# Optimization experiments

Hardware: AMD Instinct MI355X
Metric: run time of the kernel (lower is better)

## Reference

```python
import jax, jax.numpy as jnp
import numpy as np

NUM_NODES = 50000
NUM_GRAPHS = 50
HID = 128
GFD = 2
L = 4
EPS_MSG = 1e-7


def layer_norm(x, g, b, eps=1e-5):
    mu = jnp.mean(x, axis=-1, keepdims=True)
    xc = x - mu
    var = jnp.mean(xc * xc, axis=-1, keepdims=True)
    return xc * jax.lax.rsqrt(var + eps) * g + b


def gen_conv(x, src, dst, ea, t, W1, b1, g1, be1, W2, b2):
    # GENConv message: relu(x_j + edge_attr) + eps  -> [E, h]
    msg = jax.nn.relu(x[src] + ea) + EPS_MSG
    # per-destination, per-channel softmax weights of t*msg
    logits = msg * t
    m = jax.ops.segment_max(logits, dst, num_segments=NUM_NODES)
    m = jnp.where(jnp.isfinite(m), m, 0.0)  # isolated nodes -> -inf guard
    m = jax.lax.stop_gradient(m)
    ex = jnp.exp(logits - m[dst])
    s = jax.ops.segment_sum(ex, dst, num_segments=NUM_NODES)
    agg = jax.ops.segment_sum(ex * msg, dst, num_segments=NUM_NODES) / jnp.where(s > 0, s, 1.0)
    out = agg + x  # root residual inside GENConv
    # GENConv MLP: Linear(h,2h) -> LayerNorm -> ReLU -> Linear(2h,h)
    h = layer_norm(out @ W1 + b1, g1, be1)
    h = jax.nn.relu(h)
    return h @ W2 + b2


def forward(x, edge_index, edge_attr, graph_features, node_W, node_b, edge_W, edge_b,
            ts, W1s, b1s, g1s, be1s, W2s, b2s, ln_gs, ln_bs,
            head_W0, head_b0, head_W1, head_b1):
    src, dst = edge_index[0], edge_index[1]
    x = x @ node_W + node_b                 # node_encoder
    ea = edge_attr @ edge_W + edge_b        # edge_encoder
    # layers[0].conv applied directly (no pre-norm)
    x = gen_conv(x, src, dst, ea, ts[0], W1s[0], b1s[0], g1s[0], be1s[0], W2s[0], b2s[0])
    # remaining layers: res+ blocks: x = x + conv(act(norm(x)))
    for i in range(1, L):
        h = jax.nn.relu(layer_norm(x, ln_gs[i], ln_bs[i]))
        h = gen_conv(h, src, dst, ea, ts[i], W1s[i], b1s[i], g1s[i], be1s[i], W2s[i], b2s[i])
        x = x + h
    # final norm/act taken from layers[0]
    x = jax.nn.relu(layer_norm(x, ln_gs[0], ln_bs[0]))
    # dropout(p=0.1) is identity in eval mode
    # graph features broadcast to nodes (faithful reshape sequence)
    G = graph_features.shape[0]
    npg = x.shape[0] // G                   # nodes per graph
    t = jnp.repeat(graph_features.T[:, :, None], npg, axis=2)  # [gfd, G, npg]
    t = t.reshape(G, GFD, npg)              # row-major reinterpret (torch .view)
    t = jnp.transpose(t, (1, 0, 2)).reshape(GFD, G * npg)      # cat(unbind(0), dim=1)
    x = jnp.concatenate([x, t.T], axis=1)   # [N, h + gfd]
    x = jax.nn.relu(x @ head_W0 + head_b0)
    x = x @ head_W1 + head_b1
    return x


def setup_inputs() -> dict:
    key = jax.random.key(0)
    ks = jax.random.split(key, 32)
    E = 800000
    d_in, d_e = 64, 16

    def lin(k, fi, fo):
        return jax.random.normal(k, (fi, fo), jnp.float32) / np.sqrt(fi)

    inp = {
        'x': jax.random.normal(ks[0], (NUM_NODES, d_in), jnp.float32),
        'edge_index': jax.random.randint(ks[1], (2, E), 0, NUM_NODES, jnp.int64 if jax.config.jax_enable_x64 else jnp.int32),
        'edge_attr': jax.random.normal(ks[2], (E, d_e), jnp.float32),
        'graph_features': jax.random.normal(ks[3], (NUM_GRAPHS, GFD), jnp.float32),
        'node_W': lin(ks[4], d_in, HID), 'node_b': jnp.zeros((HID,), jnp.float32),
        'edge_W': lin(ks[5], d_e, HID), 'edge_b': jnp.zeros((HID,), jnp.float32),
        'ts': jnp.ones((L,), jnp.float32),
        'W1s': jnp.stack([lin(ks[6 + i], HID, 2 * HID) for i in range(L)]),
        'b1s': jnp.zeros((L, 2 * HID), jnp.float32),
        'g1s': jnp.ones((L, 2 * HID), jnp.float32),
        'be1s': jnp.zeros((L, 2 * HID), jnp.float32),
        'W2s': jnp.stack([lin(ks[10 + i], 2 * HID, HID) for i in range(L)]),
        'b2s': jnp.zeros((L, HID), jnp.float32),
        'ln_gs': jnp.ones((L, HID), jnp.float32),
        'ln_bs': jnp.zeros((L, HID), jnp.float32),
        'head_W0': lin(ks[14], HID + GFD, HID), 'head_b0': jnp.zeros((HID,), jnp.float32),
        'head_W1': lin(ks[15], HID, 1), 'head_b1': jnp.zeros((1,), jnp.float32),
    }
    return inp


def reference(x, edge_index, edge_attr, graph_features, node_W, node_b, edge_W, edge_b,
              ts, W1s, b1s, g1s, be1s, W2s, b2s, ln_gs, ln_bs,
              head_W0, head_b0, head_W1, head_b1):
    return forward(x, edge_index, edge_attr, graph_features, node_W, node_b, edge_W, edge_b,
                   ts, W1s, b1s, g1s, be1s, W2s, b2s, ln_gs, ln_bs,
                   head_W0, head_b0, head_W1, head_b1)
```

## Files before the change

kernel.cpp:

```cpp
#include <hip/hip_runtime.h>
#include <math.h>

#define EPS_MSG 1e-7f

typedef float v2f __attribute__((ext_vector_type(2)));
typedef float v4f __attribute__((ext_vector_type(4)));
typedef short bf16x8 __attribute__((ext_vector_type(8)));
typedef float f32x4 __attribute__((ext_vector_type(4)));
typedef unsigned short ush;

static __device__ inline v2f sp(float a) { v2f r; r.x = a; r.y = a; return r; }

__device__ inline unsigned short f2bf(float f) {
    union { float f; unsigned int i; } u; u.f = f;
    unsigned int b = u.i;
    return (unsigned short)((b + 0x7fffu + ((b >> 16) & 1u)) >> 16);
}
__device__ inline float bf2f(unsigned short h) {
    union { unsigned int i; float f; } u; u.i = ((unsigned int)h) << 16;
    return u.f;
}
__device__ inline v2f ubf2(unsigned int u) {
    union { unsigned int i; float f; } a, b;
    a.i = u << 16; b.i = u & 0xffff0000u;
    v2f r; r.x = a.f; r.y = b.f; return r;
}

__global__ void zero2_kernel(int* __restrict__ a, int* __restrict__ b, int n) {
    int i = blockIdx.x * 256 + threadIdx.x;
    if (i < n) { a[i] = 0; b[i] = 0; }
}

__global__ void deg_kernel(const int* __restrict__ ei, int* __restrict__ deg, int E) {
    int e = blockIdx.x * 256 + threadIdx.x;
    if (e < E) atomicAdd(&deg[ei[E + e]], 1);
}

__global__ __launch_bounds__(1024)
void scan1_kernel(const int* __restrict__ deg, int* __restrict__ offs,
                  int* __restrict__ bsum, int n) {
    __shared__ int sh[1024];
    int tid = threadIdx.x;
    int i = blockIdx.x * 1024 + tid;
    int v = (i < n) ? deg[i] : 0;
    sh[tid] = v;
    __syncthreads();
    for (int off = 1; off < 1024; off <<= 1) {
        int t = (tid >= off) ? sh[tid - off] : 0;
        __syncthreads();
        sh[tid] += t;
        __syncthreads();
    }
    if (i < n) offs[i] = sh[tid] - v;
    if (tid == 1023) bsum[blockIdx.x] = sh[tid];
}

__global__ __launch_bounds__(64)
void scan2_kernel(int* __restrict__ bsum, int nb) {
    int lane = threadIdx.x;
    int carry = 0;
    for (int base = 0; base < nb; base += 64) {
        int v = (base + lane < nb) ? bsum[base + lane] : 0;
        int incl = v;
#pragma unroll
        for (int off = 1; off < 64; off <<= 1) {
            int t = __shfl_up(incl, off, 64);
            if (lane >= off) incl += t;
        }
        if (base + lane < nb) bsum[base + lane] = incl - v + carry;
        carry += __shfl(incl, 63, 64);
    }
    if (lane == 0) bsum[nb] = carry;
}

__global__ void scan3_kernel(int* __restrict__ offs, const int* __restrict__ bsum, int n) {
    int i = blockIdx.x * 256 + threadIdx.x;
    if (i < n) offs[i] += bsum[i >> 10];
    else if (i == n) offs[n] = bsum[(n + 1023) >> 10];
}

__global__ void scatter_pos_kernel(const int* __restrict__ ei, const int* __restrict__ offs,
                                   int* __restrict__ fill, int* __restrict__ src_perm,
                                   int* __restrict__ eid_perm, int E) {
    int e = blockIdx.x * 256 + threadIdx.x;
    if (e >= E) return;
    int s = ei[e];
    int d = ei[E + e];
    int pos = offs[d] + atomicAdd(&fill[d], 1);
    src_perm[pos] = s;
    eid_perm[pos] = e;
}

__global__ void gather_attr_kernel(const float* __restrict__ edge_attr,
                                   const int* __restrict__ eid_perm,
                                   float* __restrict__ attr_perm, int E) {
    int idx = blockIdx.x * 256 + threadIdx.x;
    if (idx >= E * 4) return;
    int p = idx >> 2, c = idx & 3;
    int e = eid_perm[p];
    float4 v = *(const float4*)&edge_attr[(size_t)e * 16 + c * 4];
    *(float4*)&attr_perm[(size_t)p * 16 + c * 4] = v;
}

__global__ void wswz_kernel(const float* __restrict__ W, unsigned short* __restrict__ WH,
                            unsigned short* __restrict__ WL, int K, int Ncol, int total) {
    int idx = blockIdx.x * 256 + threadIdx.x;
    if (idx >= total) return;
    int j = idx & 7;
    int lane = (idx >> 3) & 63;
    int rest = idx >> 9;
    int ks = K >> 5;
    int kstep = rest % ks;
    int rest2 = rest / ks;
    int nc = Ncol >> 4;
    int c16 = rest2 % nc;
    int l = rest2 / nc;
    int k = kstep * 32 + (lane >> 4) * 8 + j;
    int n = c16 * 16 + (lane & 15);
    float v = W[(size_t)l * K * Ncol + (size_t)k * Ncol + n];
    unsigned short hi = f2bf(v);
    unsigned short lo = f2bf(v - bf2f(hi));
    WH[idx] = hi;
    WL[idx] = lo;
}

__global__ __launch_bounds__(256)
void encode_kernel(const float* __restrict__ x, const float* __restrict__ W,
                   const float* __restrict__ b, float* __restrict__ out,
                   unsigned short* __restrict__ xb, int N) {
    __shared__ __align__(16) float Xa[32][64];
    int tid = threadIdx.x;
    int node0 = blockIdx.x * 32;
    {
        int row = tid >> 3;
        int col = (tid & 7) * 8;
        float4 v0 = make_float4(0, 0, 0, 0), v1 = make_float4(0, 0, 0, 0);
        if (node0 + row < N) {
            const float* sp_ = &x[(size_t)(node0 + row) * 64 + col];
            v0 = *(const float4*)sp_;
            v1 = *(const float4*)(sp_ + 4);
        }
        *(float4*)&Xa[row][col] = v0;
        *(float4*)&Xa[row][col + 4] = v1;
    }
    __syncthreads();
    int tx = tid & 31, rg = tid >> 5;
    int c = tx * 4;
    v2f ba = *(const v2f*)&b[c];
    v2f bb = *(const v2f*)&b[c + 2];
    v2f acc[4][2];
#pragma unroll
    for (int i = 0; i < 4; ++i) { acc[i][0] = ba; acc[i][1] = bb; }
    for (int k = 0; k < 64; k += 4) {
        v4f W0 = *(const v4f*)&W[(k + 0) * 128 + c];
        v4f W1r = *(const v4f*)&W[(k + 1) * 128 + c];
        v4f W2r = *(const v4f*)&W[(k + 2) * 128 + c];
        v4f W3r = *(const v4f*)&W[(k + 3) * 128 + c];
#pragma unroll
        for (int i = 0; i < 4; ++i) {
            v4f xv = *(const v4f*)&Xa[rg * 4 + i][k];
            acc[i][0] = __builtin_elementwise_fma(sp(xv.x), W0.xy, acc[i][0]);
            acc[i][1] = __builtin_elementwise_fma(sp(xv.x), W0.zw, acc[i][1]);
            acc[i][0] = __builtin_elementwise_fma(sp(xv.y), W1r.xy, acc[i][0]);
            acc[i][1] = __builtin_elementwise_fma(sp(xv.y), W1r.zw, acc[i][1]);
            acc[i][0] = __builtin_elementwise_fma(sp(xv.z), W2r.xy, acc[i][0]);
            acc[i][1] = __builtin_elementwise_fma(sp(xv.z), W2r.zw, acc[i][1]);
            acc[i][0] = __builtin_elementwise_fma(sp(xv.w), W3r.xy, acc[i][0]);
            acc[i][1] = __builtin_elementwise_fma(sp(xv.w), W3r.zw, acc[i][1]);
        }
    }
#pragma unroll
    for (int i = 0; i < 4; ++i) {
        int row = node0 + rg * 4 + i;
        if (row < N) {
            float4 o = make_float4(acc[i][0].x, acc[i][0].y, acc[i][1].x, acc[i][1].y);
            *(float4*)&out[(size_t)row * 128 + c] = o;
            if (xb) {
                unsigned int u0 = (unsigned int)f2bf(o.x) | ((unsigned int)f2bf(o.y) << 16);
                unsigned int u1 = (unsigned int)f2bf(o.z) | ((unsigned int)f2bf(o.w) << 16);
                *(unsigned int*)&xb[(size_t)row * 128 + c] = u0;
                *(unsigned int*)&xb[(size_t)row * 128 + c + 2] = u1;
            }
        }
    }
}

__global__ __launch_bounds__(256)
void ln_relu_kernel(const float* __restrict__ x, const float* __restrict__ g,
                    const float* __restrict__ b, float* __restrict__ out,
                    unsigned short* __restrict__ gb, int N) {
    int lane = threadIdx.x & 63;
    int node = blockIdx.x * 4 + (threadIdx.x >> 6);
    if (node >= N) return;
    int c0 = lane * 2;
    float2 xv = *(const float2*)&x[(size_t)node * 128 + c0];
    float s = xv.x + xv.y;
    float q = xv.x * xv.x + xv.y * xv.y;
#pragma unroll
    for (int m = 1; m < 64; m <<= 1) { s += __shfl_xor(s, m, 64); q += __shfl_xor(q, m, 64); }
    float mu = s * (1.f / 128.f);
    float var = q * (1.f / 128.f) - mu * mu;
    float rs = rsqrtf(var + 1e-5f);
    float ox = fmaxf((xv.x - mu) * rs * g[c0] + b[c0], 0.f);
    float oy = fmaxf((xv.y - mu) * rs * g[c0 + 1] + b[c0 + 1], 0.f);
    float2 o; o.x = ox; o.y = oy;
    *(float2*)&out[(size_t)node * 128 + c0] = o;
    if (gb) {
        unsigned int u = (unsigned int)f2bf(ox) | ((unsigned int)f2bf(oy) << 16);
        *(unsigned int*)&gb[(size_t)node * 128 + c0] = u;
    }
}

__global__ __launch_bounds__(256)
void ln_relu_bf_kernel(const float* __restrict__ x, const float* __restrict__ g,
                       const float* __restrict__ b, unsigned short* __restrict__ outH,
                       unsigned short* __restrict__ outL, int N) {
    int lane = threadIdx.x & 63;
    int node = blockIdx.x * 4 + (threadIdx.x >> 6);
    if (node >= N) return;
    int c0 = lane * 2;
    float2 xv = *(const float2*)&x[(size_t)node * 128 + c0];
    float s = xv.x + xv.y;
    float q = xv.x * xv.x + xv.y * xv.y;
#pragma unroll
    for (int m = 1; m < 64; m <<= 1) { s += __shfl_xor(s, m, 64); q += __shfl_xor(q, m, 64); }
    float mu = s * (1.f / 128.f);
    float var = q * (1.f / 128.f) - mu * mu;
    float rs = rsqrtf(var + 1e-5f);
    float ox = fmaxf((xv.x - mu) * rs * g[c0] + b[c0], 0.f);
    float oy = fmaxf((xv.y - mu) * rs * g[c0 + 1] + b[c0 + 1], 0.f);
    unsigned short hx = f2bf(ox), hy = f2bf(oy);
    unsigned short lx = f2bf(ox - bf2f(hx)), ly = f2bf(oy - bf2f(hy));
    *(unsigned int*)&outH[(size_t)node * 128 + c0] = (unsigned int)hx | ((unsigned int)hy << 16);
    *(unsigned int*)&outL[(size_t)node * 128 + c0] = (unsigned int)lx | ((unsigned int)ly << 16);
}

template <int BF>
__global__ __launch_bounds__(128, 8)
void conv_kernel(const float* __restrict__ pre, const unsigned short* __restrict__ preb,
                 const float* __restrict__ attr_perm,
                 const int* __restrict__ src_perm, const int* __restrict__ offs,
                 const float* __restrict__ edge_W, const float* __restrict__ edge_b,
                 const float* __restrict__ ts, int layer,
                 unsigned short* __restrict__ convH, unsigned short* __restrict__ convL, int N) {
    int lane = threadIdx.x & 63;
    int node = blockIdx.x * 2 + (threadIdx.x >> 6);
    if (node >= N) return;
    int c0 = lane * 2;
    v2f wE[16];
#pragma unroll
    for (int k = 0; k < 16; ++k) {
        wE[k].x = edge_W[k * 128 + c0];
        wE[k].y = edge_W[k * 128 + c0 + 1];
    }
    v2f eb; eb.x = edge_b[c0]; eb.y = edge_b[c0 + 1];
    float t = ts[layer];
    int i0 = offs[node], i1 = offs[node + 1];
    v2f xself = *(const v2f*)&pre[(size_t)node * 128 + c0];
    float sx = 0.f, sy = 0.f, wx = 0.f, wy = 0.f;
    int i = i0;
    for (; i + 3 < i1; i += 4) {
        int iu = __builtin_amdgcn_readfirstlane(i);
        int sn0 = src_perm[iu];
        int sn1 = src_perm[iu + 1];
        int sn2 = src_perm[iu + 2];
        int sn3 = src_perm[iu + 3];
        v2f x0, x1, x2, x3;
        if (BF) {
            unsigned int u0 = *(const unsigned int*)&preb[(size_t)sn0 * 128 + c0];
            unsigned int u1 = *(const unsigned int*)&preb[(size_t)sn1 * 128 + c0];
            unsigned int u2 = *(const unsigned int*)&preb[(size_t)sn2 * 128 + c0];
            unsigned int u3 = *(const unsigned int*)&preb[(size_t)sn3 * 128 + c0];
            x0 = ubf2(u0); x1 = ubf2(u1); x2 = ubf2(u2); x3 = ubf2(u3);
        } else {
            x0 = *(const v2f*)&pre[(size_t)sn0 * 128 + c0];
            x1 = *(const v2f*)&pre[(size_t)sn1 * 128 + c0];
            x2 = *(const v2f*)&pre[(size_t)sn2 * 128 + c0];
            x3 = *(const v2f*)&pre[(size_t)sn3 * 128 + c0];
        }
        const v4f* ar = (const v4f*)(attr_perm + (size_t)iu * 16);
        v2f ea0 = eb, ea1 = eb, ea2 = eb, ea3 = eb;
#pragma unroll
        for (int k = 0; k < 4; ++k) {
            v4f A0 = ar[k];
            v4f A1 = ar[4 + k];
            v4f A2 = ar[8 + k];
            v4f A3 = ar[12 + k];
            ea0 = __builtin_elementwise_fma(sp(A0.x), wE[4 * k + 0], ea0);
            ea1 = __builtin_elementwise_fma(sp(A1.x), wE[4 * k + 0], ea1);
            ea2 = __builtin_elementwise_fma(sp(A2.x), wE[4 * k + 0], ea2);
            ea3 = __builtin_elementwise_fma(sp(A3.x), wE[4 * k + 0], ea3);
            ea0 = __builtin_elementwise_fma(sp(A0.y), wE[4 * k + 1], ea0);
            ea1 = __builtin_elementwise_fma(sp(A1.y), wE[4 * k + 1], ea1);
            ea2 = __builtin_elementwise_fma(sp(A2.y), wE[4 * k + 1], ea2);
            ea3 = __builtin_elementwise_fma(sp(A3.y), wE[4 * k + 1], ea3);
            ea0 = __builtin_elementwise_fma(sp(A0.z), wE[4 * k + 2], ea0);
            ea1 = __builtin_elementwise_fma(sp(A1.z), wE[4 * k + 2], ea1);
            ea2 = __builtin_elementwise_fma(sp(A2.z), wE[4 * k + 2], ea2);
            ea3 = __builtin_elementwise_fma(sp(A3.z), wE[4 * k + 2], ea3);
            ea0 = __builtin_elementwise_fma(sp(A0.w), wE[4 * k + 3], ea0);
            ea1 = __builtin_elementwise_fma(sp(A1.w), wE[4 * k + 3], ea1);
            ea2 = __builtin_elementwise_fma(sp(A2.w), wE[4 * k + 3], ea2);
            ea3 = __builtin_elementwise_fma(sp(A3.w), wE[4 * k + 3], ea3);
        }
        float m0x = fmaxf(x0.x + ea0.x, 0.f) + EPS_MSG;
        float m0y = fmaxf(x0.y + ea0.y, 0.f) + EPS_MSG;
        float m1x = fmaxf(x1.x + ea1.x, 0.f) + EPS_MSG;
        float m1y = fmaxf(x1.y + ea1.y, 0.f) + EPS_MSG;
        float m2x = fmaxf(x2.x + ea2.x, 0.f) + EPS_MSG;
        float m2y = fmaxf(x2.y + ea2.y, 0.f) + EPS_MSG;
        float m3x = fmaxf(x3.x + ea3.x, 0.f) + EPS_MSG;
        float m3y = fmaxf(x3.y + ea3.y, 0.f) + EPS_MSG;
        float e0x = __expf(m0x * t), e0y = __expf(m0y * t);
        float e1x = __expf(m1x * t), e1y = __expf(m1y * t);
        float e2x = __expf(m2x * t), e2y = __expf(m2y * t);
        float e3x = __expf(m3x * t), e3y = __expf(m3y * t);
        sx += (e0x + e1x) + (e2x + e3x);
        sy += (e0y + e1y) + (e2y + e3y);
        wx = fmaf(e0x, m0x, wx); wx = fmaf(e1x, m1x, wx);
        wx = fmaf(e2x, m2x, wx); wx = fmaf(e3x, m3x, wx);
        wy = fmaf(e0y, m0y, wy); wy = fmaf(e1y, m1y, wy);
        wy = fmaf(e2y, m2y, wy); wy = fmaf(e3y, m3y, wy);
    }
    for (; i < i1; ++i) {
        int iu = __builtin_amdgcn_readfirstlane(i);
        int sn = src_perm[iu];
        const v4f* ar = (const v4f*)(attr_perm + (size_t)iu * 16);
        v2f xv;
        if (BF) {
            unsigned int u = *(const unsigned int*)&preb[(size_t)sn * 128 + c0];
            xv = ubf2(u);
        } else {
            xv = *(const v2f*)&pre[(size_t)sn * 128 + c0];
        }
        v2f ea = eb;
#pragma unroll
        for (int k = 0; k < 4; ++k) {
            v4f A0 = ar[k];
            ea = __builtin_elementwise_fma(sp(A0.x), wE[4 * k + 0], ea);
            ea = __builtin_elementwise_fma(sp(A0.y), wE[4 * k + 1], ea);
            ea = __builtin_elementwise_fma(sp(A0.z), wE[4 * k + 2], ea);
            ea = __builtin_elementwise_fma(sp(A0.w), wE[4 * k + 3], ea);
        }
        float mgx = fmaxf(xv.x + ea.x, 0.f) + EPS_MSG;
        float mgy = fmaxf(xv.y + ea.y, 0.f) + EPS_MSG;
        float ex = __expf(mgx * t), ey = __expf(mgy * t);
        sx += ex; sy += ey;
        wx = fmaf(ex, mgx, wx);
        wy = fmaf(ey, mgy, wy);
    }
    float ax = (sx > 0.f) ? wx / sx : 0.f;
    float ay = (sy > 0.f) ? wy / sy : 0.f;
    float ox = ax + xself.x;
    float oy = ay + xself.y;
    unsigned short hx = f2bf(ox), hy = f2bf(oy);
    unsigned short lx = f2bf(ox - bf2f(hx)), ly = f2bf(oy - bf2f(hy));
    *(unsigned int*)&convH[(size_t)node * 128 + c0] = (unsigned int)hx | ((unsigned int)hy << 16);
    *(unsigned int*)&convL[(size_t)node * 128 + c0] = (unsigned int)lx | ((unsigned int)ly << 16);
}

template <int RES>
__global__ __launch_bounds__(256)
void mlp_mfma(const unsigned short* __restrict__ convH, const unsigned short* __restrict__ convL,
              const unsigned short* __restrict__ W1H, const unsigned short* __restrict__ W1L,
              const float* __restrict__ b1, const float* __restrict__ g1, const float* __restrict__ be1,
              const unsigned short* __restrict__ W2H, const unsigned short* __restrict__ W2L,
              const float* __restrict__ b2, const float* __restrict__ xold,
              float* __restrict__ xnew, int N) {
    __shared__ __align__(16) char SH[33792];
    __shared__ float2 ps[4][32];
    ush (*XaH)[136] = (ush(*)[136])&SH[0];
    ush (*XaL)[136] = (ush(*)[136])&SH[8704];
    ush (*XhH)[264] = (ush(*)[264])&SH[0];
    ush (*XhL)[264] = (ush(*)[264])&SH[16896];
    int tid = threadIdx.x;
    int w = tid >> 6;
    int lane = tid & 63;
    int g = lane >> 4;
    int r = lane & 15;
    int node0 = blockIdx.x * 32;
    {
        int row = tid >> 3;
        int cb = (tid & 7) * 16;
        uint4 h0 = make_uint4(0, 0, 0, 0), h1 = h0, l0 = h0, l1 = h0;
        if (node0 + row < N) {
            const uint4* pH = (const uint4*)&convH[(size_t)(node0 + row) * 128 + cb];
            const uint4* pL = (const uint4*)&convL[(size_t)(node0 + row) * 128 + cb];
            h0 = pH[0]; h1 = pH[1];
            l0 = pL[0]; l1 = pL[1];
        }
        *(uint4*)&XaH[row][cb] = h0; *(uint4*)&XaH[row][cb + 8] = h1;
        *(uint4*)&XaL[row][cb] = l0; *(uint4*)&XaL[row][cb + 8] = l1;
    }
    __syncthreads();
    f32x4 acc1[2][4];
#pragma unroll
    for (int cf = 0; cf < 4; ++cf) {
        float bv = b1[(w * 4 + cf) * 16 + r];
        f32x4 iv; iv[0] = bv; iv[1] = bv; iv[2] = bv; iv[3] = bv;
        acc1[0][cf] = iv; acc1[1][cf] = iv;
    }
#pragma unroll
    for (int kstep = 0; kstep < 4; ++kstep) {
        int ko = kstep * 32 + g * 8;
        bf16x8 aH0 = *(const bf16x8*)&XaH[r][ko];
        bf16x8 aH1 = *(const bf16x8*)&XaH[16 + r][ko];
        bf16x8 aL0 = *(const bf16x8*)&XaL[r][ko];
        bf16x8 aL1 = *(const bf16x8*)&XaL[16 + r][ko];
#pragma unroll
        for (int cf = 0; cf < 4; ++cf) {
            int c16 = w * 4 + cf;
            bf16x8 bH = *(const bf16x8*)&W1H[(((size_t)c16 * 4 + kstep) * 64 + lane) * 8];
            bf16x8 bL = *(const bf16x8*)&W1L[(((size_t)c16 * 4 + kstep) * 64 + lane) * 8];
            acc1[0][cf] = __builtin_amdgcn_mfma_f32_16x16x32_bf16(aH0, bH, acc1[0][cf], 0, 0, 0);
            acc1[0][cf] = __builtin_amdgcn_mfma_f32_16x16x32_bf16(aH0, bL, acc1[0][cf], 0, 0, 0);
            acc1[0][cf] = __builtin_amdgcn_mfma_f32_16x16x32_bf16(aL0, bH, acc1[0][cf], 0, 0, 0);
            acc1[1][cf] = __builtin_amdgcn_mfma_f32_16x16x32_bf16(aH1, bH, acc1[1][cf], 0, 0, 0);
            acc1[1][cf] = __builtin_amdgcn_mfma_f32_16x16x32_bf16(aH1, bL, acc1[1][cf], 0, 0, 0);
            acc1[1][cf] = __builtin_amdgcn_mfma_f32_16x16x32_bf16(aL1, bH, acc1[1][cf], 0, 0, 0);
        }
    }
    {
        float s_[2][4], q_[2][4];
#pragma unroll
        for (int rf = 0; rf < 2; ++rf)
#pragma unroll
            for (int reg = 0; reg < 4; ++reg) {
                float s = 0.f, q = 0.f;
#pragma unroll
                for (int cf = 0; cf < 4; ++cf) {
                    float v = acc1[rf][cf][reg];
                    s += v; q += v * v;
                }
                s_[rf][reg] = s; q_[rf][reg] = q;
            }
#pragma unroll
        for (int m = 1; m < 16; m <<= 1) {
#pragma unroll
            for (int rf = 0; rf < 2; ++rf)
#pragma unroll
                for (int reg = 0; reg < 4; ++reg) {
                    s_[rf][reg] += __shfl_xor(s_[rf][reg], m, 64);
                    q_[rf][reg] += __shfl_xor(q_[rf][reg], m, 64);
                }
        }
        if (r == 0) {
#pragma unroll
            for (int rf = 0; rf < 2; ++rf)
#pragma unroll
                for (int reg = 0; reg < 4; ++reg)
                    ps[w][rf * 16 + g * 4 + reg] = make_float2(s_[rf][reg], q_[rf][reg]);
        }
    }
    __syncthreads();
    {
        float gv[4], bev[4];
#pragma unroll
        for (int cf = 0; cf < 4; ++cf) {
            gv[cf] = g1[(w * 4 + cf) * 16 + r];
            bev[cf] = be1[(w * 4 + cf) * 16 + r];
        }
#pragma unroll
        for (int rf = 0; rf < 2; ++rf)
#pragma unroll
            for (int reg = 0; reg < 4; ++reg) {
                int row = rf * 16 + g * 4 + reg;
                float2 t0 = ps[0][row], t1 = ps[1][row], t2 = ps[2][row], t3 = ps[3][row];
                float s = t0.x + t1.x + t2.x + t3.x;
                float q = t0.y + t1.y + t2.y + t3.y;
                float mu = s * (1.f / 256.f);
                float var = q * (1.f / 256.f) - mu * mu;
                float rs = rsqrtf(var + 1e-5f);
#pragma unroll
                for (int cf = 0; cf < 4; ++cf) {
                    float h = fmaxf((acc1[rf][cf][reg] - mu) * rs * gv[cf] + bev[cf], 0.f);
                    unsigned short hh = f2bf(h);
                    unsigned short hl = f2bf(h - bf2f(hh));
                    int col = (w * 4 + cf) * 16 + r;
                    XhH[row][col] = hh;
                    XhL[row][col] = hl;
                }
            }
    }
    __syncthreads();
    f32x4 acc2[2][2];
#pragma unroll
    for (int cf = 0; cf < 2; ++cf) {
        float bv = b2[(w * 2 + cf) * 16 + r];
        f32x4 iv; iv[0] = bv; iv[1] = bv; iv[2] = bv; iv[3] = bv;
        acc2[0][cf] = iv; acc2[1][cf] = iv;
    }
#pragma unroll
    for (int kstep = 0; kstep < 8; ++kstep) {
        int ko = kstep * 32 + g * 8;
        bf16x8 aH0 = *(const bf16x8*)&XhH[r][ko];
        bf16x8 aH1 = *(const bf16x8*)&XhH[16 + r][ko];
        bf16x8 aL0 = *(const bf16x8*)&XhL[r][ko];
        bf16x8 aL1 = *(const bf16x8*)&XhL[16 + r][ko];
#pragma unroll
        for (int cf = 0; cf < 2; ++cf) {
            int c16 = w * 2 + cf;
            bf16x8 bH = *(const bf16x8*)&W2H[(((size_t)c16 * 8 + kstep) * 64 + lane) * 8];
            bf16x8 bL = *(const bf16x8*)&W2L[(((size_t)c16 * 8 + kstep) * 64 + lane) * 8];
            acc2[0][cf] = __builtin_amdgcn_mfma_f32_16x16x32_bf16(aH0, bH, acc2[0][cf], 0, 0, 0);
            acc2[0][cf] = __builtin_amdgcn_mfma_f32_16x16x32_bf16(aH0, bL, acc2[0][cf], 0, 0, 0);
            acc2[0][cf] = __builtin_amdgcn_mfma_f32_16x16x32_bf16(aL0, bH, acc2[0][cf], 0, 0, 0);
            acc2[1][cf] = __builtin_amdgcn_mfma_f32_16x16x32_bf16(aH1, bH, acc2[1][cf], 0, 0, 0);
            acc2[1][cf] = __builtin_amdgcn_mfma_f32_16x16x32_bf16(aH1, bL, acc2[1][cf], 0, 0, 0);
            acc2[1][cf] = __builtin_amdgcn_mfma_f32_16x16x32_bf16(aL1, bH, acc2[1][cf], 0, 0, 0);
        }
    }
#pragma unroll
    for (int rf = 0; rf < 2; ++rf)
#pragma unroll
        for (int reg = 0; reg < 4; ++reg) {
            int row = node0 + rf * 16 + g * 4 + reg;
            if (row < N) {
#pragma unroll
                for (int cf = 0; cf < 2; ++cf) {
                    int col = (w * 2 + cf) * 16 + r;
                    float v = acc2[rf][cf][reg];
                    if (RES) v += xold[(size_t)row * 128 + col];
                    xnew[(size_t)row * 128 + col] = v;
                }
            }
        }
}

__global__ __launch_bounds__(256)
void head_mfma(const unsigned short* __restrict__ PREH, const unsigned short* __restrict__ PREL,
               const unsigned short* __restrict__ W0H, const unsigned short* __restrict__ W0L,
               const float* __restrict__ W0, const float* __restrict__ b0,
               const float* __restrict__ gf, const float* __restrict__ W1h,
               const float* __restrict__ b1h, float* __restrict__ out, int N) {
    __shared__ __align__(16) unsigned short XH[32][136];
    __shared__ __align__(16) unsigned short XL[32][136];
    __shared__ float gf0s[32], gf1s[32];
    __shared__ float psum[4][32];
    int tid = threadIdx.x;
    int w = tid >> 6;
    int lane = tid & 63;
    int g = lane >> 4;
    int r = lane & 15;
    int node0 = blockIdx.x * 32;
    {
        int row = tid >> 3;
        int cb = (tid & 7) * 16;
        uint4 h0 = make_uint4(0, 0, 0, 0), h1 = h0, l0 = h0, l1 = h0;
        if (node0 + row < N) {
            const uint4* pH = (const uint4*)&PREH[(size_t)(node0 + row) * 128 + cb];
            const uint4* pL = (const uint4*)&PREL[(size_t)(node0 + row) * 128 + cb];
            h0 = pH[0]; h1 = pH[1];
            l0 = pL[0]; l1 = pL[1];
        }
        *(uint4*)&XH[row][cb] = h0; *(uint4*)&XH[row][cb + 8] = h1;
        *(uint4*)&XL[row][cb] = l0; *(uint4*)&XL[row][cb + 8] = l1;
        if (tid < 32) {
            int node = node0 + tid;
            float f0 = 0.f, f1 = 0.f;
            if (node < N) {
                int a = node / 1000;
                int i0 = 2 * a, i1 = 2 * a + 1;
                f0 = (i0 < 50) ? gf[i0 * 2] : gf[(i0 - 50) * 2 + 1];
                f1 = (i1 < 50) ? gf[i1 * 2] : gf[(i1 - 50) * 2 + 1];
            }
            gf0s[tid] = f0;
            gf1s[tid] = f1;
        }
    }
    __syncthreads();
    f32x4 acc[2][2];
#pragma unroll
    for (int cf = 0; cf < 2; ++cf) {
        float bv = b0[(w * 2 + cf) * 16 + r];
        f32x4 iv; iv[0] = bv; iv[1] = bv; iv[2] = bv; iv[3] = bv;
        acc[0][cf] = iv; acc[1][cf] = iv;
    }
#pragma unroll
    for (int kstep = 0; kstep < 4; ++kstep) {
        int ko = kstep * 32 + g * 8;
        bf16x8 aH0 = *(const bf16x8*)&XH[r][ko];
        bf16x8 aH1 = *(const bf16x8*)&XH[16 + r][ko];
        bf16x8 aL0 = *(const bf16x8*)&XL[r][ko];
        bf16x8 aL1 = *(const bf16x8*)&XL[16 + r][ko];
#pragma unroll
        for (int cf = 0; cf < 2; ++cf) {
            int c16 = w * 2 + cf;
            bf16x8 bH = *(const bf16x8*)&W0H[(((size_t)c16 * 4 + kstep) * 64 + lane) * 8];
            bf16x8 bL = *(const bf16x8*)&W0L[(((size_t)c16 * 4 + kstep) * 64 + lane) * 8];
            acc[0][cf] = __builtin_amdgcn_mfma_f32_16x16x32_bf16(aH0, bH, acc[0][cf], 0, 0, 0);
            acc[0][cf] = __builtin_amdgcn_mfma_f32_16x16x32_bf16(aH0, bL, acc[0][cf], 0, 0, 0);
            acc[0][cf] = __builtin_amdgcn_mfma_f32_16x16x32_bf16(aL0, bH, acc[0][cf], 0, 0, 0);
            acc[1][cf] = __builtin_amdgcn_mfma_f32_16x16x32_bf16(aH1, bH, acc[1][cf], 0, 0, 0);
            acc[1][cf] = __builtin_amdgcn_mfma_f32_16x16x32_bf16(aH1, bL, acc[1][cf], 0, 0, 0);
            acc[1][cf] = __builtin_amdgcn_mfma_f32_16x16x32_bf16(aL1, bH, acc[1][cf], 0, 0, 0);
        }
    }
    {
        float w1v[2], wg0[2], wg1[2];
#pragma unroll
        for (int cf = 0; cf < 2; ++cf) {
            int col = (w * 2 + cf) * 16 + r;
            w1v[cf] = W1h[col];
            wg0[cf] = W0[128 * 128 + col];
            wg1[cf] = W0[129 * 128 + col];
        }
#pragma unroll
        for (int rf = 0; rf < 2; ++rf)
#pragma unroll
            for (int reg = 0; reg < 4; ++reg) {
                int rowl = rf * 16 + g * 4 + reg;
                float f0 = gf0s[rowl], f1 = gf1s[rowl];
                float p = 0.f;
#pragma unroll
                for (int cf = 0; cf < 2; ++cf) {
                    float v = acc[rf][cf][reg] + f0 * wg0[cf] + f1 * wg1[cf];
                    v = fmaxf(v, 0.f);
                    p = fmaf(v, w1v[cf], p);
                }
#pragma unroll
                for (int m = 1; m < 16; m <<= 1) p += __shfl_xor(p, m, 64);
                if (r == 0) psum[w][rowl] = p;
            }
    }
    __syncthreads();
    if (tid < 32) {
        int node = node0 + tid;
        if (node < N) {
            float s = psum[0][tid] + psum[1][tid] + psum[2][tid] + psum[3][tid] + b1h[0];
            out[node] = s;
        }
    }
}

extern "C" void kernel_launch(void* const* d_in, const int* in_sizes, int n_in,
                              void* d_out, int out_size, void* d_ws, size_t ws_size,
                              hipStream_t stream) {
    const float* x_in    = (const float*)d_in[0];
    const int*   ei      = (const int*)d_in[1];
    const float* edge_attr = (const float*)d_in[2];
    const float* gf      = (const float*)d_in[3];
    const float* node_W  = (const float*)d_in[4];
    const float* node_b  = (const float*)d_in[5];
    const float* edge_W  = (const float*)d_in[6];
    const float* edge_b  = (const float*)d_in[7];
    const float* ts      = (const float*)d_in[8];
    const float* W1s     = (const float*)d_in[9];
    const float* b1s     = (const float*)d_in[10];
    const float* g1s     = (const float*)d_in[11];
    const float* be1s    = (const float*)d_in[12];
    const float* W2s     = (const float*)d_in[13];
    const float* b2s     = (const float*)d_in[14];
    const float* ln_gs   = (const float*)d_in[15];
    const float* ln_bs   = (const float*)d_in[16];
    const float* hW0     = (const float*)d_in[17];
    const float* hb0     = (const float*)d_in[18];
    const float* hW1     = (const float*)d_in[19];
    const float* hb1     = (const float*)d_in[20];

    const int N = in_sizes[0] / 64;
    const int E = in_sizes[1] / 2;
    const int NB = (N + 1023) / 1024;

    char* ws = (char*)d_ws;
    size_t off = 0;
    auto alloc = [&](size_t bytes) -> void* {
        void* p = ws + off;
        off = (off + bytes + 255) & ~(size_t)255;
        return p;
    };
    float* X     = (float*)alloc((size_t)N * 128 * 4);
    float* PRE   = (float*)alloc((size_t)N * 128 * 4);
    unsigned short* CONVH = (unsigned short*)alloc((size_t)N * 128 * 2);
    unsigned short* CONVL = (unsigned short*)alloc((size_t)N * 128 * 2);
    unsigned short* W1H = (unsigned short*)alloc((size_t)4 * 128 * 256 * 2);
    unsigned short* W1L = (unsigned short*)alloc((size_t)4 * 128 * 256 * 2);
    unsigned short* W2H = (unsigned short*)alloc((size_t)4 * 256 * 128 * 2);
    unsigned short* W2L = (unsigned short*)alloc((size_t)4 * 256 * 128 * 2);
    int* SRCP    = (int*)alloc((size_t)E * 4);
    int* DEG     = (int*)alloc((size_t)N * 4);
    int* FILL    = (int*)alloc((size_t)N * 4);
    int* OFFS    = (int*)alloc((size_t)(N + 1) * 4);
    int* BSUM    = (int*)alloc((size_t)(NB + 1) * 4);
    float* ATTRP = (float*)alloc((size_t)E * 16 * 4);

    unsigned short* GB = (unsigned short*)(ws + off);
    int mode_bf = (off + (size_t)N * 128 * 2 <= ws_size) ? 1 : 0;
    if (!mode_bf) GB = nullptr;

    unsigned short* W0H = (unsigned short*)DEG;
    unsigned short* W0L = W0H + 128 * 128;
    int* EIDP = (int*)CONVH;

    const int TOT = 4 * 128 * 256;
    wswz_kernel<<<(TOT + 255) / 256, 256, 0, stream>>>(W1s, W1H, W1L, 128, 256, TOT);
    wswz_kernel<<<(TOT + 255) / 256, 256, 0, stream>>>(W2s, W2H, W2L, 256, 128, TOT);

    zero2_kernel<<<(N + 255) / 256, 256, 0, stream>>>(DEG, FILL, N);
    deg_kernel<<<(E + 255) / 256, 256, 0, stream>>>(ei, DEG, E);
    scan1_kernel<<<NB, 1024, 0, stream>>>(DEG, OFFS, BSUM, N);
    scan2_kernel<<<1, 64, 0, stream>>>(BSUM, NB);
    scan3_kernel<<<(N + 256) / 256, 256, 0, stream>>>(OFFS, BSUM, N);
    scatter_pos_kernel<<<(E + 255) / 256, 256, 0, stream>>>(ei, OFFS, FILL, SRCP, EIDP, E);
    gather_attr_kernel<<<(E * 4 + 255) / 256, 256, 0, stream>>>(edge_attr, EIDP, ATTRP, E);
    wswz_kernel<<<(128 * 128 + 255) / 256, 256, 0, stream>>>(hW0, W0H, W0L, 128, 128, 128 * 128);

    encode_kernel<<<(N + 31) / 32, 256, 0, stream>>>(x_in, node_W, node_b, X, GB, N);

    for (int layer = 0; layer < 4; ++layer) {
        const float* pre = X;
        if (layer > 0) {
            ln_relu_kernel<<<(N + 3) / 4, 256, 0, stream>>>(X, ln_gs + 128 * layer, ln_bs + 128 * layer,
                                                            PRE, GB, N);
            pre = PRE;
        }
        if (mode_bf)
            conv_kernel<1><<<(N + 1) / 2, 128, 0, stream>>>(pre, GB, ATTRP, SRCP, OFFS, edge_W, edge_b,
                                                            ts, layer, CONVH, CONVL, N);
        else
            conv_kernel<0><<<(N + 1) / 2, 128, 0, stream>>>(pre, nullptr, ATTRP, SRCP, OFFS, edge_W, edge_b,
                                                            ts, layer, CONVH, CONVL, N);
        const unsigned short* w1h = W1H + (size_t)layer * 128 * 256;
        const unsigned short* w1l = W1L + (size_t)layer * 128 * 256;
        const unsigned short* w2h = W2H + (size_t)layer * 256 * 128;
        const unsigned short* w2l = W2L + (size_t)layer * 256 * 128;
        if (layer == 0)
            mlp_mfma<0><<<(N + 31) / 32, 256, 0, stream>>>(CONVH, CONVL, w1h, w1l,
                                                           b1s + layer * 256, g1s + layer * 256, be1s + layer * 256,
                                                           w2h, w2l, b2s + layer * 128, X, X, N);
        else
            mlp_mfma<1><<<(N + 31) / 32, 256, 0, stream>>>(CONVH, CONVL, w1h, w1l,
                                                           b1s + layer * 256, g1s + layer * 256, be1s + layer * 256,
                                                           w2h, w2l, b2s + layer * 128, X, X, N);
    }

    ln_relu_bf_kernel<<<(N + 3) / 4, 256, 0, stream>>>(X, ln_gs, ln_bs, CONVH, CONVL, N);
    head_mfma<<<(N + 31) / 32, 256, 0, stream>>>(CONVH, CONVL, W0H, W0L, hW0, hb0, gf, hW1, hb1,
                                                 (float*)d_out, N);
}
```

Before: 690.9 us.

## Fuse layer-norm+ReLU epilogue into MLP kernel and drop separate LN kernels

The MLP kernel epilogue now computes the row-wise layer norm and ReLU for the next layer using a shuffle reduction plus a shared-memory cross-wave reduction. It writes PRE and the bf16 copy, or on the last layer the hi/lo bf16 split consumed by the head. This removes the standalone ln_relu and ln_relu_bf kernels and their extra read of X. The bf16 gather buffer is now always allocated, so the fallback path without it is gone. The epilogue adds a __syncthreads and uncoalesced scalar 2-byte stores.

```diff
diff --git a/kernel.cpp b/kernel.cpp
--- a/kernel.cpp
+++ b/kernel.cpp
@@ -175,64 +175,12 @@
         if (row < N) {
             float4 o = make_float4(acc[i][0].x, acc[i][0].y, acc[i][1].x, acc[i][1].y);
             *(float4*)&out[(size_t)row * 128 + c] = o;
-            if (xb) {
-                unsigned int u0 = (unsigned int)f2bf(o.x) | ((unsigned int)f2bf(o.y) << 16);
-                unsigned int u1 = (unsigned int)f2bf(o.z) | ((unsigned int)f2bf(o.w) << 16);
-                *(unsigned int*)&xb[(size_t)row * 128 + c] = u0;
-                *(unsigned int*)&xb[(size_t)row * 128 + c + 2] = u1;
-            }
-        }
-    }
-}
-
-__global__ __launch_bounds__(256)
-void ln_relu_kernel(const float* __restrict__ x, const float* __restrict__ g,
-                    const float* __restrict__ b, float* __restrict__ out,
-                    unsigned short* __restrict__ gb, int N) {
-    int lane = threadIdx.x & 63;
-    int node = blockIdx.x * 4 + (threadIdx.x >> 6);
-    if (node >= N) return;
-    int c0 = lane * 2;
-    float2 xv = *(const float2*)&x[(size_t)node * 128 + c0];
-    float s = xv.x + xv.y;
-    float q = xv.x * xv.x + xv.y * xv.y;
-#pragma unroll
-    for (int m = 1; m < 64; m <<= 1) { s += __shfl_xor(s, m, 64); q += __shfl_xor(q, m, 64); }
-    float mu = s * (1.f / 128.f);
-    float var = q * (1.f / 128.f) - mu * mu;
-    float rs = rsqrtf(var + 1e-5f);
-    float ox = fmaxf((xv.x - mu) * rs * g[c0] + b[c0], 0.f);
-    float oy = fmaxf((xv.y - mu) * rs * g[c0 + 1] + b[c0 + 1], 0.f);
-    float2 o; o.x = ox; o.y = oy;
-    *(float2*)&out[(size_t)node * 128 + c0] = o;
-    if (gb) {
-        unsigned int u = (unsigned int)f2bf(ox) | ((unsigned int)f2bf(oy) << 16);
-        *(unsigned int*)&gb[(size_t)node * 128 + c0] = u;
-    }
-}
-
-__global__ __launch_bounds__(256)
-void ln_relu_bf_kernel(const float* __restrict__ x, const float* __restrict__ g,
-                       const float* __restrict__ b, unsigned short* __restrict__ outH,
-                       unsigned short* __restrict__ outL, int N) {
-    int lane = threadIdx.x & 63;
-    int node = blockIdx.x * 4 + (threadIdx.x >> 6);
-    if (node >= N) return;
-    int c0 = lane * 2;
-    float2 xv = *(const float2*)&x[(size_t)node * 128 + c0];
-    float s = xv.x + xv.y;
-    float q = xv.x * xv.x + xv.y * xv.y;
-#pragma unroll
-    for (int m = 1; m < 64; m <<= 1) { s += __shfl_xor(s, m, 64); q += __shfl_xor(q, m, 64); }
-    float mu = s * (1.f / 128.f);
-    float var = q * (1.f / 128.f) - mu * mu;
-    float rs = rsqrtf(var + 1e-5f);
-    float ox = fmaxf((xv.x - mu) * rs * g[c0] + b[c0], 0.f);
-    float oy = fmaxf((xv.y - mu) * rs * g[c0 + 1] + b[c0 + 1], 0.f);
-    unsigned short hx = f2bf(ox), hy = f2bf(oy);
-    unsigned short lx = f2bf(ox - bf2f(hx)), ly = f2bf(oy - bf2f(hy));
-    *(unsigned int*)&outH[(size_t)node * 128 + c0] = (unsigned int)hx | ((unsigned int)hy << 16);
-    *(unsigned int*)&outL[(size_t)node * 128 + c0] = (unsigned int)lx | ((unsigned int)ly << 16);
+            unsigned int u0 = (unsigned int)f2bf(o.x) | ((unsigned int)f2bf(o.y) << 16);
+            unsigned int u1 = (unsigned int)f2bf(o.z) | ((unsigned int)f2bf(o.w) << 16);
+            *(unsigned int*)&xb[(size_t)row * 128 + c] = u0;
+            *(unsigned int*)&xb[(size_t)row * 128 + c + 2] = u1;
+        }
+    }
 }
 
 template <int BF>
@@ -359,14 +307,16 @@
     *(unsigned int*)&convL[(size_t)node * 128 + c0] = (unsigned int)lx | ((unsigned int)ly << 16);
 }
 
-template <int RES>
+template <int RES, int MODE>
 __global__ __launch_bounds__(256)
-void mlp_mfma(const unsigned short* __restrict__ convH, const unsigned short* __restrict__ convL,
+void mlp_mfma(const unsigned short* __restrict__ convH_c, const unsigned short* __restrict__ convL_c,
               const unsigned short* __restrict__ W1H, const unsigned short* __restrict__ W1L,
               const float* __restrict__ b1, const float* __restrict__ g1, const float* __restrict__ be1,
               const unsigned short* __restrict__ W2H, const unsigned short* __restrict__ W2L,
               const float* __restrict__ b2, const float* __restrict__ xold,
-              float* __restrict__ xnew, int N) {
+              float* __restrict__ xnew, const float* __restrict__ lng, const float* __restrict__ lnb,
+              float* __restrict__ preo, unsigned short* __restrict__ gbo,
+              unsigned short* __restrict__ convH, unsigned short* __restrict__ convL, int N) {
     __shared__ __align__(16) char SH[33792];
     __shared__ float2 ps[4][32];
     ush (*XaH)[136] = (ush(*)[136])&SH[0];
@@ -384,8 +334,8 @@
         int cb = (tid & 7) * 16;
         uint4 h0 = make_uint4(0, 0, 0, 0), h1 = h0, l0 = h0, l1 = h0;
         if (node0 + row < N) {
-            const uint4* pH = (const uint4*)&convH[(size_t)(node0 + row) * 128 + cb];
-            const uint4* pL = (const uint4*)&convL[(size_t)(node0 + row) * 128 + cb];
+            const uint4* pH = (const uint4*)&convH_c[(size_t)(node0 + row) * 128 + cb];
+            const uint4* pL = (const uint4*)&convL_c[(size_t)(node0 + row) * 128 + cb];
             h0 = pH[0]; h1 = pH[1];
             l0 = pL[0]; l1 = pL[1];
         }
@@ -510,21 +460,79 @@
             acc2[1][cf] = __builtin_amdgcn_mfma_f32_16x16x32_bf16(aL1, bH, acc2[1][cf], 0, 0, 0);
         }
     }
+    float vv[2][4][2];
 #pragma unroll
     for (int rf = 0; rf < 2; ++rf)
 #pragma unroll
         for (int reg = 0; reg < 4; ++reg) {
             int row = node0 + rf * 16 + g * 4 + reg;
-            if (row < N) {
+#pragma unroll
+            for (int cf = 0; cf < 2; ++cf) {
+                int col = (w * 2 + cf) * 16 + r;
+                float v = acc2[rf][cf][reg];
+                if (RES && row < N) v += xold[(size_t)row * 128 + col];
+                vv[rf][reg][cf] = v;
+                if (MODE == 0 && row < N) xnew[(size_t)row * 128 + col] = v;
+            }
+        }
+    {
+        float s_[2][4], q_[2][4];
+#pragma unroll
+        for (int rf = 0; rf < 2; ++rf)
+#pragma unroll
+            for (int reg = 0; reg < 4; ++reg) {
+                float s = vv[rf][reg][0] + vv[rf][reg][1];
+                float q = vv[rf][reg][0] * vv[rf][reg][0] + vv[rf][reg][1] * vv[rf][reg][1];
+#pragma unroll
+                for (int m = 1; m < 16; m <<= 1) { s += __shfl_xor(s, m, 64); q += __shfl_xor(q, m, 64); }
+                s_[rf][reg] = s; q_[rf][reg] = q;
+            }
+        if (r == 0) {
+#pragma unroll
+            for (int rf = 0; rf < 2; ++rf)
+#pragma unroll
+                for (int reg = 0; reg < 4; ++reg)
+                    ps[w][rf * 16 + g * 4 + reg] = make_float2(s_[rf][reg], q_[rf][reg]);
+        }
+    }
+    __syncthreads();
+    {
+        float lg[2], lb[2];
+#pragma unroll
+        for (int cf = 0; cf < 2; ++cf) {
+            int col = (w * 2 + cf) * 16 + r;
+            lg[cf] = lng[col];
+            lb[cf] = lnb[col];
+        }
+#pragma unroll
+        for (int rf = 0; rf < 2; ++rf)
+#pragma unroll
+            for (int reg = 0; reg < 4; ++reg) {
+                int rowl = rf * 16 + g * 4 + reg;
+                int row = node0 + rowl;
+                if (row >= N) continue;
+                float2 t0 = ps[0][rowl], t1 = ps[1][rowl], t2 = ps[2][rowl], t3 = ps[3][rowl];
+                float s = t0.x + t1.x + t2.x + t3.x;
+                float q = t0.y + t1.y + t2.y + t3.y;
+                float mu = s * (1.f / 128.f);
+                float var = q * (1.f / 128.f) - mu * mu;
+                float rs = rsqrtf(var + 1e-5f);
 #pragma unroll
                 for (int cf = 0; cf < 2; ++cf) {
                     int col = (w * 2 + cf) * 16 + r;
-                    float v = acc2[rf][cf][reg];
-                    if (RES) v += xold[(size_t)row * 128 + col];
-                    xnew[(size_t)row * 128 + col] = v;
+                    float h = fmaxf((vv[rf][reg][cf] - mu) * rs * lg[cf] + lb[cf], 0.f);
+                    if (MODE == 0) {
+                        preo[(size_t)row * 128 + col] = h;
+                        gbo[(size_t)row * 128 + col] = f2bf(h);
+                    } else {
+                        unsigned short hh = f2bf(h);
+                        unsigned short hl = f2bf(h - bf2f(hh));
+                        convH[(size_t)row * 128 + col] = hh;
+                        convL[(size_t)row * 128 + col] = hl;
+                    }
                 }
             }
-        }
+    }
 }
 
 __global__ __launch_bounds__(256)
@@ -673,6 +681,7 @@
     float* PRE   = (float*)alloc((size_t)N * 128 * 4);
     unsigned short* CONVH = (unsigned short*)alloc((size_t)N * 128 * 2);
     unsigned short* CONVL = (unsigned short*)alloc((size_t)N * 128 * 2);
+    unsigned short* GB = (unsigned short*)alloc((size_t)N * 128 * 2);
     unsigned short* W1H = (unsigned short*)alloc((size_t)4 * 128 * 256 * 2);
     unsigned short* W1L = (unsigned short*)alloc((size_t)4 * 128 * 256 * 2);
     unsigned short* W2H = (unsigned short*)alloc((size_t)4 * 256 * 128 * 2);
@@ -684,10 +693,6 @@
     int* BSUM    = (int*)alloc((size_t)(NB + 1) * 4);
     float* ATTRP = (float*)alloc((size_t)E * 16 * 4);
 
-    unsigned short* GB = (unsigned short*)(ws + off);
-    int mode_bf = (off + (size_t)N * 128 * 2 <= ws_size) ? 1 : 0;
-    if (!mode_bf) GB = nullptr;
-
     unsigned short* W0H = (unsigned short*)DEG;
     unsigned short* W0L = W0H + 128 * 128;
     int* EIDP = (int*)CONVH;
@@ -708,33 +713,29 @@
     encode_kernel<<<(N + 31) / 32, 256, 0, stream>>>(x_in, node_W, node_b, X, GB, N);
 
     for (int layer = 0; layer < 4; ++layer) {
-        const float* pre = X;
-        if (layer > 0) {
-            ln_relu_kernel<<<(N + 3) / 4, 256, 0, stream>>>(X, ln_gs + 128 * layer, ln_bs + 128 * layer,
-                                                            PRE, GB, N);
-            pre = PRE;
-        }
-        if (mode_bf)
-            conv_kernel<1><<<(N + 1) / 2, 128, 0, stream>>>(pre, GB, ATTRP, SRCP, OFFS, edge_W, edge_b,
-                                                            ts, layer, CONVH, CONVL, N);
-        else
-            conv_kernel<0><<<(N + 1) / 2, 128, 0, stream>>>(pre, nullptr, ATTRP, SRCP, OFFS, edge_W, edge_b,
-                                                            ts, layer, CONVH, CONVL, N);
+        const float* pre = (layer == 0) ? X : PRE;
+        conv_kernel<1><<<(N + 1) / 2, 128, 0, stream>>>(pre, GB, ATTRP, SRCP, OFFS, edge_W, edge_b,
+                                                        ts, layer, CONVH, CONVL, N);
         const unsigned short* w1h = W1H + (size_t)layer * 128 * 256;
         const unsigned short* w1l = W1L + (size_t)layer * 128 * 256;
         const unsigned short* w2h = W2H + (size_t)layer * 256 * 128;
         const unsigned short* w2l = W2L + (size_t)layer * 256 * 128;
+        const float* lng = (layer < 3) ? (ln_gs + 128 * (layer + 1)) : ln_gs;
+        const float* lnb = (layer < 3) ? (ln_bs + 128 * (layer + 1)) : ln_bs;
         if (layer == 0)
-            mlp_mfma<0><<<(N + 31) / 32, 256, 0, stream>>>(CONVH, CONVL, w1h, w1l,
-                                                           b1s + layer * 256, g1s + layer * 256, be1s + layer * 256,
-                                                           w2h, w2l, b2s + layer * 128, X, X, N);
+            mlp_mfma<0, 0><<<(N + 31) / 32, 256, 0, stream>>>(CONVH, CONVL, w1h, w1l,
+                b1s + layer * 256, g1s + layer * 256, be1s + layer * 256,
+                w2h, w2l, b2s + layer * 128, X, X, lng, lnb, PRE, GB, CONVH, CONVL, N);
+        else if (layer < 3)
+            mlp_mfma<1, 0><<<(N + 31) / 32, 256, 0, stream>>>(CONVH, CONVL, w1h, w1l,
+                b1s + layer * 256, g1s + layer * 256, be1s + layer * 256,
+                w2h, w2l, b2s + layer * 128, X, X, lng, lnb, PRE, GB, CONVH, CONVL, N);
         else
-            mlp_mfma<1><<<(N + 31) / 32, 256, 0, stream>>>(CONVH, CONVL, w1h, w1l,
-                                                           b1s + layer * 256, g1s + layer * 256, be1s + layer * 256,
-                                                           w2h, w2l, b2s + layer * 128, X, X, N);
-    }
-
-    ln_relu_bf_kernel<<<(N + 3) / 4, 256, 0, stream>>>(X, ln_gs, ln_bs, CONVH, CONVL, N);
+            mlp_mfma<1, 1><<<(N + 31) / 32, 256, 0, stream>>>(CONVH, CONVL, w1h, w1l,
+                b1s + layer * 256, g1s + layer * 256, be1s + layer * 256,
+                w2h, w2l, b2s + layer * 128, X, X, lng, lnb, PRE, GB, CONVH, CONVL, N);
+    }
+
     head_mfma<<<(N + 31) / 32, 256, 0, stream>>>(CONVH, CONVL, W0H, W0L, hW0, hb0, gf, hW1, hb1,
                                                  (float*)d_out, N);
 }
```

Result: faster. 673.7 us, median of 2 (-2.5%).
